# Kernel optimization log

Hardware: AMD Instinct MI355X
Metric: run time of the kernel (lower is better)

Reference implementation:

```python
import jax, jax.numpy as jnp
import numpy as np

K_NEIGH = 12
RADIUS = 0.5


def _mlp(x, w1, b1, w2, b2):
    return jax.nn.relu(x @ w1 + b1) @ w2 + b2


def _angle(a, b):
    # atan2(||a x b||, a.b), as in PyG point-pair features
    c = jnp.cross(a, b)
    return jnp.arctan2(jnp.linalg.norm(c, axis=-1), jnp.sum(a * b, axis=-1))


def _quat_to_mat(q):
    w, x, y, z = q[:, 0], q[:, 1], q[:, 2], q[:, 3]
    m = jnp.stack([
        1 - 2 * (y * y + z * z), 2 * (x * y - z * w), 2 * (x * z + y * w),
        2 * (x * y + z * w), 1 - 2 * (x * x + z * z), 2 * (y * z - x * w),
        2 * (x * z - y * w), 2 * (y * z + x * w), 1 - 2 * (x * x + y * y),
    ], axis=-1)
    return m.reshape(-1, 3, 3)


def _lin_params(key, fan_in, fan_out):
    kw, kb = jax.random.split(key)
    s = 1.0 / np.sqrt(fan_in)
    w = jax.random.uniform(kw, (fan_in, fan_out), minval=-s, maxval=s, dtype=jnp.float32)
    b = jax.random.uniform(kb, (fan_out,), minval=-s, maxval=s, dtype=jnp.float32)
    return w, b


def setup_inputs() -> dict:
    key = jax.random.key(0)
    keys = jax.random.split(key, 8)
    points = jax.random.uniform(keys[0], (1, 128, 64, 3), dtype=jnp.float32)
    dims = [(7, 32, 16), (19, 32, 8), (24, 32, 16), (16, 32, 8), (24, 32, 16), (16, 32, 12), (27, 64, 1)]
    names = ['l1', 'g1', 'l2', 'g2', 'l3', 'g3', 'l4']
    inp = {'points': points}
    for i, (nm, (di, dh, do)) in enumerate(zip(names, dims)):
        k1, k2 = jax.random.split(keys[i + 1])
        w1, b1 = _lin_params(k1, di, dh)
        w2, b2 = _lin_params(k2, dh, do)
        inp[nm + '_w1'], inp[nm + '_b1'], inp[nm + '_w2'], inp[nm + '_b2'] = w1, b1, w2, b2
    return inp


def reference(points, l1_w1, l1_b1, l1_w2, l1_b2, g1_w1, g1_b1, g1_w2, g1_b2,
              l2_w1, l2_b1, l2_w2, l2_b2, g2_w1, g2_b1, g2_w2, g2_b2,
              l3_w1, l3_b1, l3_w2, l3_b2, g3_w1, g3_b1, g3_w2, g3_b2,
              l4_w1, l4_b1, l4_w2, l4_b2):
    B, H, W, _ = points.shape
    pos = points.reshape(-1, 3)          # [N,3]
    N = pos.shape[0]
    K = K_NEIGH
    pos_sg = jax.lax.stop_gradient(pos)  # torch detaches pos before edge features

    # --- dense radius graph: K nearest neighbors, self-padded beyond radius ---
    sq = jnp.sum(pos_sg * pos_sg, -1)
    d2 = sq[:, None] + sq[None, :] - 2.0 * (pos_sg @ pos_sg.T)  # [N,N]
    idx = jnp.arange(N)
    d2 = d2.at[idx, idx].set(jnp.inf)
    neg_d2_k, knn = jax.lax.top_k(-d2, K)
    d2_k = -neg_d2_k
    dense = jnp.where(d2_k <= RADIUS * RADIUS, knn, idx[:, None])  # [N,K]
    rows = jnp.repeat(idx, K)            # [E]
    cols = dense.reshape(-1)             # [E]

    # --- covariance of neighborhood, analytic 3x3 eig -> PCA normals ---
    nbr = pos[dense]                     # [N,K,3] (non-detached, as in torch)
    cent = jnp.mean(nbr, axis=1, keepdims=True)
    diff = nbr - cent
    cov = jnp.einsum('nki,nkj->nij', diff, diff) / K
    noise = (jax.random.uniform(jax.random.key(42), (100, 3), dtype=jnp.float32) - 0.5) * 1e-8
    cov = cov + jnp.diag(noise)          # torch.diag of (100,3) -> length-3 vector broadcast
    eig_val, eig_vec = jnp.linalg.eigh(cov)  # ascending, matches sort+gather in torch
    normals = eig_vec[:, :, 0]           # eigenvector of smallest eigenvalue
    pca_normals = normals.reshape(B, H, W, 3).transpose(0, 3, 1, 2)

    # --- edge feature stack: gather-MLP-mean-broadcast chain ---
    cart = pos_sg[cols] - pos_sg[rows]   # [E,3]
    dist = jnp.linalg.norm(cart, axis=-1)
    n_r, n_c = normals[rows], normals[cols]
    ppf = jnp.stack([dist, _angle(n_r, cart), _angle(n_c, cart), _angle(n_r, n_c)], -1)
    x = _mlp(jnp.concatenate([cart, ppf], -1), l1_w1, l1_b1, l1_w2, l1_b2)  # [E,16]

    gx = jnp.concatenate([x.reshape(N, K, -1).mean(1), normals], -1)        # [N,19]
    x_g = _mlp(gx, g1_w1, g1_b1, g1_w2, g1_b2)                              # [N,8]
    x = _mlp(jnp.concatenate([x, x_g[rows]], 1), l2_w1, l2_b1, l2_w2, l2_b2)

    x_g = _mlp(x.reshape(N, K, -1).mean(1), g2_w1, g2_b1, g2_w2, g2_b2)
    x = _mlp(jnp.concatenate([x, x_g[rows]], 1), l3_w1, l3_b1, l3_w2, l3_b2)

    x_g = _mlp(x.reshape(N, K, -1).mean(1), g3_w1, g3_b1, g3_w2, g3_b2)     # [N,12]
    quat = x_g[:, :4]
    quat = quat / (jnp.linalg.norm(quat, axis=-1) + 1e-8)[:, None]
    mat = _quat_to_mat(quat)             # [N,3,3]
    feat_g = x_g[:, 4:]
    rot_cart = jnp.einsum('eij,ej->ei', mat[rows], cart)
    x = _mlp(jnp.concatenate([x, feat_g[rows], rot_cart], 1), l4_w1, l4_b1, l4_w2, l4_b2)

    point_fea = jax.nn.softmax(x.reshape(N, K), axis=1)
    point_fea = point_fea.reshape(B, H, W, K).transpose(0, 3, 1, 2)
    return pca_normals, point_fea
```

## Files before the change

kernel.cpp:

```cpp
#include <hip/hip_runtime.h>
#include <math.h>

#define KNB 12
#define GRD 8
#define NCELL (GRD * GRD * GRD)


__device__ __forceinline__ unsigned umin32(unsigned a, unsigned b) {
    unsigned r; asm("v_min_u32 %0, %1, %2" : "=v"(r) : "v"(a), "v"(b)); return r;
}
__device__ __forceinline__ unsigned umax32(unsigned a, unsigned b) {
    unsigned r; asm("v_max_u32 %0, %1, %2" : "=v"(r) : "v"(a), "v"(b)); return r;
}

__device__ __forceinline__ float fm(float a, float b) { return __fmul_rn(a, b); }
__device__ __forceinline__ float fa(float a, float b) { return __fadd_rn(a, b); }
__device__ __forceinline__ float fs(float a, float b) { return __fsub_rn(a, b); }
__device__ __forceinline__ float fsignf(float a, float b) { return (b >= 0.0f) ? fabsf(a) : -fabsf(a); }

__device__ float slapy2_(float x, float y) {
    float xa = fabsf(x), ya = fabsf(y);
    float w = fmaxf(xa, ya), z = fminf(xa, ya);
    if (z == 0.0f) return w;
    float q = z / w;
    return fm(w, __fsqrt_rn(fa(1.0f, fm(q, q))));
}

__device__ void slartg_(float f, float g, float& c, float& s, float& r) {
    if (g == 0.0f) { c = 1.0f; s = 0.0f; r = f; }
    else if (f == 0.0f) { c = 0.0f; s = (g >= 0.0f) ? 1.0f : -1.0f; r = fabsf(g); }
    else {
        float d = __fsqrt_rn(fa(fm(f, f), fm(g, g)));
        c = fabsf(f) / d;
        r = (f >= 0.0f) ? d : -d;
        s = g / r;
    }
}

__device__ void slaev2_(float a, float b, float cc,
                        float& rt1, float& rt2, float& cs1, float& sn1) {
    float sm = fa(a, cc), df = fs(a, cc), adf = fabsf(df);
    float tb = fa(b, b), ab = fabsf(tb);
    float acmx, acmn;
    if (fabsf(a) > fabsf(cc)) { acmx = a; acmn = cc; } else { acmx = cc; acmn = a; }
    float rt;
    if (adf > ab)      { float q = ab / adf; rt = fm(adf, __fsqrt_rn(fa(1.0f, fm(q, q)))); }
    else if (adf < ab) { float q = adf / ab; rt = fm(ab,  __fsqrt_rn(fa(1.0f, fm(q, q)))); }
    else               rt = fm(ab, __fsqrt_rn(2.0f));
    int sgn1;
    if (sm < 0.0f) {
        rt1 = fm(0.5f, fs(sm, rt)); sgn1 = -1;
        rt2 = fs(fm(acmx / rt1, acmn), fm(b / rt1, b));
    } else if (sm > 0.0f) {
        rt1 = fm(0.5f, fa(sm, rt)); sgn1 = 1;
        rt2 = fs(fm(acmx / rt1, acmn), fm(b / rt1, b));
    } else { rt1 = fm(0.5f, rt); rt2 = fm(-0.5f, rt); sgn1 = 1; }
    int sgn2; float cs;
    if (df >= 0.0f) { cs = fa(df, rt); sgn2 = 1; } else { cs = fs(df, rt); sgn2 = -1; }
    float acs = fabsf(cs);
    if (acs > ab) {
        float ct = -tb / cs;
        sn1 = 1.0f / __fsqrt_rn(fa(1.0f, fm(ct, ct)));
        cs1 = fm(ct, sn1);
    } else {
        if (ab == 0.0f) { cs1 = 1.0f; sn1 = 0.0f; }
        else {
            float tn = -cs / tb;
            cs1 = 1.0f / __fsqrt_rn(fa(1.0f, fm(tn, tn)));
            sn1 = fm(tn, cs1);
        }
    }
    if (sgn1 == sgn2) { float tn = cs1; cs1 = -sn1; sn1 = tn; }
}

__device__ __forceinline__ void rot2col(float& a1, float& a2, float& a3,
                                        float& b1, float& b2, float& b3,
                                        float ct, float st) {
    float t;
    t = b1; b1 = fs(fm(ct, t), fm(st, a1)); a1 = fa(fm(st, t), fm(ct, a1));
    t = b2; b2 = fs(fm(ct, t), fm(st, a2)); a2 = fa(fm(st, t), fm(ct, a2));
    t = b3; b3 = fs(fm(ct, t), fm(st, a3)); a3 = fa(fm(st, t), fm(ct, a3));
}

#define RD(i)    ((i) == 1 ? d1 : ((i) == 2 ? d2 : d3))
#define WRD(i,v) do { float _t = (v); if ((i) == 1) d1 = _t; else if ((i) == 2) d2 = _t; else d3 = _t; } while (0)
#define RE(i)    ((i) == 1 ? e1 : e2)
#define WRE(i,v) do { float _t = (v); if ((i) == 1) e1 = _t; else e2 = _t; } while (0)
#define SWAPC(a,b) do { float _t = (a); (a) = (b); (b) = _t; } while (0)

__device__ void eig3_smallest_reg(float a00, float a10, float a20,
                                  float a11, float a21, float a22,
                                  float& v1o, float& v2o, float& v3o) {
    float z11 = 1.0f, z21 = 0.0f, z31 = 0.0f;
    float z12 = 0.0f, z22 = 1.0f, z32 = 0.0f;
    float z13 = 0.0f, z23 = 0.0f, z33 = 1.0f;
    float d1, d2, d3, e1, e2;
    float wc1 = 0.0f, wc2 = 0.0f, ws1 = 0.0f, ws2 = 0.0f;

    float tau = 0.0f, v3 = 0.0f;
    d1 = a00;
    if (a20 != 0.0f) {
        float xn = fabsf(a20);
        float beta = -fsignf(slapy2_(a10, xn), a10);
        tau = fs(beta, a10) / beta;
        float rinv = 1.0f / fs(a10, beta);
        v3 = fm(a20, rinv);
        e1 = beta;
        float w1 = fa(fm(tau, a11), fm(tau, fm(a21, v3)));
        float w2 = fa(fm(tau, a21), fm(fm(tau, v3), a22));
        float dot = fa(w1, fm(w2, v3));
        float al = fm(fm(-0.5f, tau), dot);
        w1 = fa(w1, al);
        w2 = fa(w2, fm(al, v3));
        d2 = fs(fs(a11, w1), w1);
        e2 = fs(fs(a21, fm(v3, w1)), w2);
        d3 = fs(fs(a22, fm(v3, w2)), fm(w2, v3));
    } else {
        e1 = a10; d2 = a11; e2 = a21; d3 = a22;
    }

    const float eps = 5.9604645e-8f;
    const float eps2 = 3.5527137e-15f;
    const float safmin = 1.17549435e-38f;
    int jtot = 0; const int nmaxit = 90;
    int l1 = 1;
    while (l1 <= 3) {
        if (l1 > 1) WRE(l1 - 1, 0.0f);
        int m;
        for (m = l1; m <= 2; ++m) {
            float tst = fabsf(RE(m));
            if (tst == 0.0f) break;
            if (tst <= fm(fm(__fsqrt_rn(fabsf(RD(m))), __fsqrt_rn(fabsf(RD(m + 1)))), eps)) {
                WRE(m, 0.0f); break;
            }
        }
        int l = l1, lend = m;
        l1 = m + 1;
        if (lend == l) continue;
        if (fabsf(RD(lend)) < fabsf(RD(l))) { int t = l; l = lend; lend = t; }
        if (lend > l) {
            for (;;) {
                int mq = lend;
                if (l != lend) {
                    for (mq = l; mq <= lend - 1; ++mq) {
                        float tst = fm(RE(mq), RE(mq));
                        if (tst <= fa(fm(fm(eps2, fabsf(RD(mq))), fabsf(RD(mq + 1))), safmin)) break;
                    }
                }
                if (mq < lend) WRE(mq, 0.0f);
                float p = RD(l);
                if (mq == l) { l += 1; if (l <= lend) continue; break; }
                if (mq == l + 1) {
                    float rt1, rt2, cc, ss;
                    if (l == 1) {
                        slaev2_(d1, e1, d2, rt1, rt2, cc, ss);
                        rot2col(z11, z21, z31, z12, z22, z32, cc, ss);
                        d1 = rt1; d2 = rt2; e1 = 0.0f;
                    } else {
                        slaev2_(d2, e2, d3, rt1, rt2, cc, ss);
                        rot2col(z12, z22, z32, z13, z23, z33, cc, ss);
                        d2 = rt1; d3 = rt2; e2 = 0.0f;
                    }
                    l += 2; if (l <= lend) continue; break;
                }
                if (jtot == nmaxit) break;
                jtot++;
                float g = fs(d2, p) / fm(2.0f, e1);
                float r = slapy2_(g, 1.0f);
                g = fa(fs(d3, p), e1 / fa(g, fsignf(r, g)));
                float s_ = 1.0f, c_ = 1.0f; p = 0.0f;
                {
                    float f = fm(s_, e2), b = fm(c_, e2);
                    slartg_(g, f, c_, s_, r);
                    g = fs(d3, p);
                    r = fa(fm(fs(d2, g), s_), fm(fm(2.0f, c_), b));
                    p = fm(s_, r);
                    d3 = fa(g, p);
                    g = fs(fm(c_, r), b);
                    wc2 = c_; ws2 = -s_;
                }
                {
                    float f = fm(s_, e1), b = fm(c_, e1);
                    slartg_(g, f, c_, s_, r);
                    e2 = r;
                    g = fs(d2, p);
                    r = fa(fm(fs(d1, g), s_), fm(fm(2.0f, c_), b));
                    p = fm(s_, r);
                    d2 = fa(g, p);
                    g = fs(fm(c_, r), b);
                    wc1 = c_; ws1 = -s_;
                }
                rot2col(z12, z22, z32, z13, z23, z33, wc2, ws2);
                rot2col(z11, z21, z31, z12, z22, z32, wc1, ws1);
                d1 = fs(d1, p); e1 = g;
            }
        } else {
            for (;;) {
                int mq = lend;
                if (l != lend) {
                    for (mq = l; mq >= lend + 1; --mq) {
                        float tst = fm(RE(mq - 1), RE(mq - 1));
                        if (tst <= fa(fm(fm(eps2, fabsf(RD(mq))), fabsf(RD(mq - 1))), safmin)) break;
                    }
                }
                if (mq > lend) WRE(mq - 1, 0.0f);
                float p = RD(l);
                if (mq == l) { l -= 1; if (l >= lend) continue; break; }
                if (mq == l - 1) {
                    float rt1, rt2, cc, ss;
                    if (l == 2) {
                        slaev2_(d1, e1, d2, rt1, rt2, cc, ss);
                        rot2col(z11, z21, z31, z12, z22, z32, cc, ss);
                        d1 = rt1; d2 = rt2; e1 = 0.0f;
                    } else {
                        slaev2_(d2, e2, d3, rt1, rt2, cc, ss);
                        rot2col(z12, z22, z32, z13, z23, z33, cc, ss);
                        d2 = rt1; d3 = rt2; e2 = 0.0f;
                    }
                    l -= 2; if (l >= lend) continue; break;
                }
                if (jtot == nmaxit) break;
                jtot++;
                float g = fs(d2, p) / fm(2.0f, e2);
                float r = slapy2_(g, 1.0f);
                g = fa(fs(d1, p), e2 / fa(g, fsignf(r, g)));
                float s_ = 1.0f, c_ = 1.0f; p = 0.0f;
                {
                    float f = fm(s_, e1), b = fm(c_, e1);
                    slartg_(g, f, c_, s_, r);
                    g = fs(d1, p);
                    r = fa(fm(fs(d2, g), s_), fm(fm(2.0f, c_), b));
                    p = fm(s_, r);
                    d1 = fa(g, p);
                    g = fs(fm(c_, r), b);
                    wc1 = c_; ws1 = s_;
                }
                {
                    float f = fm(s_, e2), b = fm(c_, e2);
                    slartg_(g, f, c_, s_, r);
                    e1 = r;
                    g = fs(d2, p);
                    r = fa(fm(fs(d3, g), s_), fm(fm(2.0f, c_), b));
                    p = fm(s_, r);
                    d2 = fa(g, p);
                    g = fs(fm(c_, r), b);
                    wc2 = c_; ws2 = s_;
                }
                rot2col(z11, z21, z31, z12, z22, z32, wc1, ws1);
                rot2col(z12, z22, z32, z13, z23, z33, wc2, ws2);
                d3 = fs(d3, p); e2 = g;
            }
        }
    }
    for (int ii = 2; ii <= 3; ++ii) {
        int i = ii - 1, kk = i; float p = RD(i);
        for (int j = ii; j <= 3; ++j) { float dj = RD(j); if (dj < p) { kk = j; p = dj; } }
        if (kk != i) {
            WRD(kk, RD(i)); WRD(i, p);
            if (i == 1 && kk == 2)      { SWAPC(z11, z12); SWAPC(z21, z22); SWAPC(z31, z32); }
            else if (i == 1 && kk == 3) { SWAPC(z11, z13); SWAPC(z21, z23); SWAPC(z31, z33); }
            else                        { SWAPC(z12, z13); SWAPC(z22, z23); SWAPC(z32, z33); }
        }
    }
    if (tau != 0.0f) {
        float ss, t;
        ss = fa(z21, fm(v3, z31)); t = fm(tau, ss); z21 = fs(z21, t); z31 = fs(z31, fm(t, v3));
        ss = fa(z22, fm(v3, z32)); t = fm(tau, ss); z22 = fs(z22, t); z32 = fs(z32, fm(t, v3));
        ss = fa(z23, fm(v3, z33)); t = fm(tau, ss); z23 = fs(z23, t); z33 = fs(z33, fm(t, v3));
    }
    v1o = z11; v2o = z21; v3o = z31;
}

__device__ void threefry2x32_(unsigned k0, unsigned k1, unsigned c0, unsigned c1,
                              unsigned& o0, unsigned& o1) {
    const unsigned rot[8] = {13u, 15u, 26u, 6u, 17u, 29u, 16u, 24u};
    unsigned ks[3] = {k0, k1, k0 ^ k1 ^ 0x1BD11BDAu};
    unsigned x0 = c0 + k0, x1 = c1 + k1;
    for (int blk = 0; blk < 5; ++blk) {
        const unsigned* r = &rot[(blk & 1) * 4];
        for (int i = 0; i < 4; ++i) {
            x0 += x1;
            x1 = (x1 << r[i]) | (x1 >> (32 - r[i]));
            x1 ^= x0;
        }
        x0 += ks[(blk + 1) % 3];
        x1 += ks[(blk + 2) % 3] + (unsigned)(blk + 1);
    }
    o0 = x0; o1 = x1;
}

__device__ float noise_diag_(int j) {
    unsigned m = (unsigned)(4 * j);
    unsigned o0, o1;
    threefry2x32_(0u, 42u, m, 150u + m, o0, o1);
    unsigned bits = (o0 >> 9) | 0x3f800000u;
    float u = fs(__uint_as_float(bits), 1.0f);
    return fm(fs(u, 0.5f), 1e-8f);
}

__device__ __forceinline__ float angf(float ax, float ay, float az,
                                      float bx, float by, float bz) {
    float cx = ay * bz - az * by;
    float cy = az * bx - ax * bz;
    float cz = ax * by - ay * bx;
    float cn = sqrtf(cx * cx + cy * cy + cz * cz);
    float d  = ax * bx + ay * by + az * bz;
    return atan2f(cn, d);
}

__global__ __launch_bounds__(1024) void k_build(const float* __restrict__ pts,
                                                float4* __restrict__ pos4,
                                                int* __restrict__ order,
                                                int* __restrict__ start, int n) {
    __shared__ int sh[NCELL];
    __shared__ int scur[NCELL];
    int t = threadIdx.x;

    for (int c = t; c < NCELL; c += 1024) sh[c] = 0;
    __syncthreads();

    for (int i = t; i < n; i += 1024) {
        float x = pts[i * 3], y = pts[i * 3 + 1], z = pts[i * 3 + 2];
        float sq = fa(fa(fm(x, x), fm(y, y)), fm(z, z));
        pos4[i] = make_float4(x, y, z, sq);
        int cx = (int)(x * 8.0f); cx = cx < 0 ? 0 : (cx > GRD - 1 ? GRD - 1 : cx);
        int cy = (int)(y * 8.0f); cy = cy < 0 ? 0 : (cy > GRD - 1 ? GRD - 1 : cy);
        int cz = (int)(z * 8.0f); cz = cz < 0 ? 0 : (cz > GRD - 1 ? GRD - 1 : cz);
        int cid = (cz * GRD + cy) * GRD + cx;
        atomicAdd(&sh[cid], 1);
    }
    __syncthreads();

    int v = 0;
    if (t < NCELL) v = sh[t];
    for (int off = 1; off < NCELL; off <<= 1) {
        int x = 0;
        if (t < NCELL && t >= off) x = sh[t - off];
        __syncthreads();
        if (t < NCELL) sh[t] += x;
        __syncthreads();
    }
    if (t < NCELL) {
        int ex = sh[t] - v;
        start[t] = ex;
        scur[t] = ex;
        if (t == NCELL - 1) start[NCELL] = sh[t];
    }
    __syncthreads();

    for (int i = t; i < n; i += 1024) {
        float4 P = pos4[i];
        int cx = (int)(P.x * 8.0f); cx = cx < 0 ? 0 : (cx > GRD - 1 ? GRD - 1 : cx);
        int cy = (int)(P.y * 8.0f); cy = cy < 0 ? 0 : (cy > GRD - 1 ? GRD - 1 : cy);
        int cz = (int)(P.z * 8.0f); cz = cz < 0 ? 0 : (cz > GRD - 1 ? GRD - 1 : cz);
        int cid = (cz * GRD + cy) * GRD + cx;
        int slot = atomicAdd(&scur[cid], 1);
        order[slot] = i;
    }
}

#define KEY_WORST 0xC0001FFFFFFFFFFFull
#define CBUF 128

__global__ __launch_bounds__(256) void k_knn(const float4* __restrict__ pos4,
                                             const int* __restrict__ order,
                                             const int* __restrict__ cstart,
                                             int* __restrict__ cols,
                                             float4* __restrict__ nrm4,
                                             float* __restrict__ out, int n) {
    __shared__ unsigned long long sbuf[4][CBUF];
    __shared__ int scnt[4];
    __shared__ float4 sq4[4][KNB];

    int lane = threadIdx.x & 63;
    int wv = threadIdx.x >> 6;
    int io = blockIdx.x * 4 + wv;
    bool wact = (io < n);

    if (wact) {
        float4 P = pos4[io];
        int cx = (int)(P.x * 8.0f); cx = cx < 0 ? 0 : (cx > GRD - 1 ? GRD - 1 : cx);
        int cy = (int)(P.y * 8.0f); cy = cy < 0 ? 0 : (cy > GRD - 1 ? GRD - 1 : cy);
        int cz = (int)(P.z * 8.0f); cz = cz < 0 ? 0 : (cz > GRD - 1 ? GRD - 1 : cz);

        unsigned T = 0xFFFFFFFFu;
        int xlo = 0, xhi = 0, ylo = 0, yhi = 0, zlo = 0, zhi = 0;

        for (int r = 1; r < 16; ++r) {
            xlo = cx - r; if (xlo < 0) xlo = 0;
            xhi = cx + r; if (xhi > GRD - 1) xhi = GRD - 1;
            ylo = cy - r; if (ylo < 0) ylo = 0;
            yhi = cy + r; if (yhi > GRD - 1) yhi = GRD - 1;
            zlo = cz - r; if (zlo < 0) zlo = 0;
            zhi = cz + r; if (zhi > GRD - 1) zhi = GRD - 1;

            unsigned b0 = 0xFFFFFFFFu, b1 = 0xFFFFFFFFu;
            for (int zz = zlo; zz <= zhi; ++zz)
                for (int yy = ylo; yy <= yhi; ++yy) {
                    int rowb = (zz * GRD + yy) * GRD;
                    int jb = cstart[rowb + xlo];
                    int je = cstart[rowb + xhi + 1];
                    for (int t = jb + lane; t < je; t += 64) {
                        int j = order[t];
                        float4 Q = pos4[j];
                        float g = fm(P.x, Q.x);
                        g = fmaf(P.y, Q.y, g);
                        g = fmaf(P.z, Q.z, g);
                        float d2 = fs(fa(P.w, Q.w), fm(2.0f, g));
                        unsigned u = __float_as_uint(d2);
                        u = (j == io) ? 0xFFFFFFFFu : u;
                        unsigned lo = umin32(b0, u);
                        unsigned hi = umax32(b0, u);
                        b0 = lo;
                        b1 = umin32(b1, hi);
                    }
                }

            {
                unsigned h0 = b0, h1 = b1;
                T = 0xFFFFFFFFu;
                for (int rr = 0; rr < KNB + 1; ++rr) {
                    unsigned mn = h0;
#pragma unroll
                    for (int off = 32; off >= 1; off >>= 1) {
                        unsigned o = (unsigned)__shfl_xor((int)mn, off, 64);
                        mn = umin32(mn, o);
                    }
                    unsigned long long bl = __ballot(h0 == mn);
                    int first = __ffsll(bl) - 1;
                    if (lane == first) { h0 = h1; h1 = 0xFFFFFFFFu; }
                    T = mn;
                }
            }

            bool cover = (xlo == 0) && (xhi == GRD - 1) && (ylo == 0) && (yhi == GRD - 1)
                      && (zlo == 0) && (zhi == GRD - 1);
            if (cover) break;
            if (T != 0xFFFFFFFFu) {
                float gmin = 1e30f;
                if (xlo > 0)       gmin = fminf(gmin, fs(P.x, (float)xlo * 0.125f));
                if (xhi < GRD - 1) gmin = fminf(gmin, fs((float)(xhi + 1) * 0.125f, P.x));
                if (ylo > 0)       gmin = fminf(gmin, fs(P.y, (float)ylo * 0.125f));
                if (yhi < GRD - 1) gmin = fminf(gmin, fs((float)(yhi + 1) * 0.125f, P.y));
                if (zlo > 0)       gmin = fminf(gmin, fs(P.z, (float)zlo * 0.125f));
                if (zhi < GRD - 1) gmin = fminf(gmin, fs((float)(zhi + 1) * 0.125f, P.z));
                float g2 = fm(fm(gmin, gmin), 0.9995f);
                if (__uint_as_float(T) <= g2) break;
            }
        }

        if (lane == 0) scnt[wv] = 0;
        __builtin_amdgcn_wave_barrier();
        for (int zz = zlo; zz <= zhi; ++zz)
            for (int yy = ylo; yy <= yhi; ++yy) {
                int rowb = (zz * GRD + yy) * GRD;
                int jb = cstart[rowb + xlo];
                int je = cstart[rowb + xhi + 1];
                for (int t = jb + lane; t < je; t += 64) {
                    int j = order[t];
                    float4 Q = pos4[j];
                    float g = fm(P.x, Q.x);
                    g = fmaf(P.y, Q.y, g);
                    g = fmaf(P.z, Q.z, g);
                    float d2 = fs(fa(P.w, Q.w), fm(2.0f, g));
                    unsigned u = __float_as_uint(d2);
                    bool c = (u <= T) && (j != io);
                    unsigned long long bl = __ballot(c);
                    if (bl) {
                        int leader = __ffsll(bl) - 1;
                        int base = 0;
                        if (lane == leader)
                            base = atomicAdd(&scnt[wv], (int)__popcll(bl));
                        base = __shfl(base, leader, 64);
                        if (c) {
                            int pos = base + (int)__popcll(bl & ((1ull << lane) - 1ull));
                            unsigned us = u ^ (unsigned)(((int)u >> 31) | 0x80000000);
                            unsigned long long kb = (((unsigned long long)us << 13) | (unsigned)j)
                                                    | 0xC000000000000000ull;
                            if (pos < CBUF) sbuf[wv][pos] = kb;
                        }
                    }
                }
            }
        __builtin_amdgcn_wave_barrier();
        int cnt = scnt[wv];
        if (cnt > CBUF) cnt = CBUF;

        double k0 = __longlong_as_double((long long)KEY_WORST);
        double k1 = __longlong_as_double((long long)KEY_WORST);
        if (lane < cnt) k0 = __longlong_as_double((long long)sbuf[wv][lane]);
        if (lane + 64 < cnt) k1 = __longlong_as_double((long long)sbuf[wv][lane + 64]);
        double mykey = __longlong_as_double((long long)KEY_WORST);
        for (int rr = 0; rr < KNB; ++rr) {
            double mx = fmax(k0, k1);
#pragma unroll
            for (int off = 32; off >= 1; off >>= 1)
                mx = fmax(mx, __shfl_xor(mx, off, 64));
            if (k0 == mx) k0 = __longlong_as_double((long long)KEY_WORST);
            else if (k1 == mx) k1 = __longlong_as_double((long long)KEY_WORST);
            if (lane == rr) mykey = mx;
        }
        if (lane < KNB) {
            unsigned long long bits = (unsigned long long)__double_as_longlong(mykey);
            unsigned j = (unsigned)(bits & 0x1FFFu);
            unsigned u = (unsigned)((bits >> 13) & 0xFFFFFFFFull);
            unsigned ob = (u & 0x80000000u) ? (u ^ 0x80000000u) : ~u;
            float d2 = __uint_as_float(ob);
            int cv = (d2 <= 0.25f) ? (int)j : io;
            cols[io * KNB + lane] = cv;
            float4 qp = pos4[cv];
            sq4[wv][lane] = make_float4(qp.x, qp.y, qp.z, 0.0f);
        }
    }
    __syncthreads();

    if (wv == 0 && lane < 4) {
        int pp = blockIdx.x * 4 + lane;
        if (pp < n) {
            float qx[KNB], qy[KNB], qz[KNB];
#pragma unroll
            for (int k = 0; k < KNB; ++k) {
                float4 q = sq4[lane][k];
                qx[k] = q.x; qy[k] = q.y; qz[k] = q.z;
            }
            float sx = qx[0], sy = qy[0], sz = qz[0];
#pragma unroll
            for (int k = 1; k < KNB; ++k) { sx = fa(sx, qx[k]); sy = fa(sy, qy[k]); sz = fa(sz, qz[k]); }
            float mx = sx / 12.0f, my = sy / 12.0f, mz = sz / 12.0f;
            float c00 = 0, c10 = 0, c20 = 0, c11 = 0, c21 = 0, c22 = 0;
#pragma unroll
            for (int k = 0; k < KNB; ++k) {
                float dx = fs(qx[k], mx), dy = fs(qy[k], my), dz = fs(qz[k], mz);
                c00 = fa(c00, fm(dx, dx));
                c10 = fa(c10, fm(dy, dx));
                c20 = fa(c20, fm(dz, dx));
                c11 = fa(c11, fm(dy, dy));
                c21 = fa(c21, fm(dz, dy));
                c22 = fa(c22, fm(dz, dz));
            }
            c00 = c00 / 12.0f; c10 = c10 / 12.0f; c20 = c20 / 12.0f;
            c11 = c11 / 12.0f; c21 = c21 / 12.0f; c22 = c22 / 12.0f;
            float v0 = noise_diag_(0), v1 = noise_diag_(1), v2 = noise_diag_(2);
            float a00 = fa(c00, v0), a10 = fa(c10, v0), a20 = fa(c20, v0);
            float a11 = fa(c11, v1), a21 = fa(c21, v1), a22 = fa(c22, v2);
            float e1, e2, e3;
            eig3_smallest_reg(a00, a10, a20, a11, a21, a22, e1, e2, e3);
            nrm4[pp] = make_float4(e1, e2, e3, 0.0f);
            out[pp]         = e1;
            out[n + pp]     = e2;
            out[2 * n + pp] = e3;
        }
    }
}


struct WPtrs { const float* p[28]; };

template <int NI, int NH, int NO>
__device__ __forceinline__ void mlp_half(const float* __restrict__ w1, const float* __restrict__ b1,
                                         const float* __restrict__ w2, const float* __restrict__ b2,
                                         const float* in, float* out, int hf) {
#pragma unroll
    for (int o = 0; o < NO; ++o) out[o] = hf ? 0.0f : b2[o];
    const int HH = NH / 2;
    int h0 = hf * HH;
    for (int hi = 0; hi < HH; ++hi) {
        int h = h0 + hi;
        float hh = b1[h];
#pragma unroll
        for (int ii = 0; ii < NI; ++ii) hh = fmaf(in[ii], w1[ii * NH + h], hh);
        hh = fmaxf(hh, 0.0f);
#pragma unroll
        for (int o = 0; o < NO; ++o) out[o] = fmaf(hh, w2[h * NO + o], out[o]);
    }
}

template <int NI, int NO>
__device__ __forceinline__ void gmlp_part(const float* __restrict__ w1, const float* __restrict__ b1,
                                          const float* __restrict__ w2, const float* __restrict__ b2,
                                          const float* in, float* pout, int q) {
#pragma unroll
    for (int o = 0; o < NO; ++o) pout[o] = (q == 0) ? b2[o] : 0.0f;
    {
        float hh = b1[q];
#pragma unroll
        for (int ii = 0; ii < NI; ++ii) hh = fmaf(in[ii], w1[ii * 32 + q], hh);
        hh = fmaxf(hh, 0.0f);
#pragma unroll
        for (int o = 0; o < NO; ++o) pout[o] = fmaf(hh, w2[q * NO + o], pout[o]);
    }
    if (q < 8) {
        int h = 24 + q;
        float hh = b1[h];
#pragma unroll
        for (int ii = 0; ii < NI; ++ii) hh = fmaf(in[ii], w1[ii * 32 + h], hh);
        hh = fmaxf(hh, 0.0f);
#pragma unroll
        for (int o = 0; o < NO; ++o) pout[o] = fmaf(hh, w2[h * NO + o], pout[o]);
    }
}

#define SCR(pp, qq, oo) s_scr[((pp) * 24 + (qq)) * 17 + (oo)]
#define SM(pp, oo)      s_m[(pp) * 17 + (oo)]
#define GFV(pp, oo)     s_g[(pp) * 13 + (oo)]
#define SLG(pp, kk)     s_log[(pp) * 13 + (kk)]

__global__ __launch_bounds__(384) void k_mlp(const float4* __restrict__ pos4,
                                             const int* __restrict__ cols,
                                             const float4* __restrict__ nrm4,
                                             WPtrs wp, float* __restrict__ out, int n) {
    __shared__ float s_scr[16 * 24 * 17];
    __shared__ float s_m[16 * 17];
    __shared__ float s_g[16 * 13];
    __shared__ float s_log[16 * 13];
    __shared__ float s_red[16 * 2];

    int t = threadIdx.x;
    int tm = t % 192;
    int p = tm / 12, k = tm - p * 12;
    int hf = __builtin_amdgcn_readfirstlane(t / 192);
    int q = hf * 12 + k;
    int nn = blockIdx.x * 16 + p;
    bool act = (nn < n);

    float cx = 0, cy = 0, cz = 0, nrx = 0, nry = 0, nrz = 0;
    float xr[16];

    if (act) {
        int col = cols[nn * 12 + k];
        float4 P = pos4[nn], Q = pos4[col];
        cx = Q.x - P.x; cy = Q.y - P.y; cz = Q.z - P.z;
        float dist = sqrtf(cx * cx + cy * cy + cz * cz);
        float4 NR = nrm4[nn], NC = nrm4[col];
        nrx = NR.x; nry = NR.y; nrz = NR.z;
        float a1 = angf(nrx, nry, nrz, cx, cy, cz);
        float a2 = angf(NC.x, NC.y, NC.z, cx, cy, cz);
        float a3 = angf(nrx, nry, nrz, NC.x, NC.y, NC.z);
        float in7[7] = {cx, cy, cz, dist, a1, a2, a3};
        float px[16];
        mlp_half<7, 32, 16>(wp.p[0], wp.p[1], wp.p[2], wp.p[3], in7, px, hf);
#pragma unroll
        for (int o = 0; o < 16; ++o) SCR(p, q, o) = px[o];
    }
    __syncthreads();
    if (act) {
#pragma unroll
        for (int o = 0; o < 16; ++o) xr[o] = SCR(p, k, o) + SCR(p, 12 + k, o);
    }
    __syncthreads();

    if (act && q < 16) {
        float s = 0.0f;
        for (int kk = 0; kk < 12; ++kk) s += SCR(p, kk, q) + SCR(p, 12 + kk, q);
        SM(p, q) = s / 12.0f;
    }
    __syncthreads();
    if (act) {
        float gin[19];
#pragma unroll
        for (int ii = 0; ii < 16; ++ii) gin[ii] = SM(p, ii);
        gin[16] = nrx; gin[17] = nry; gin[18] = nrz;
        float pg[8];
        gmlp_part<19, 8>(wp.p[4], wp.p[5], wp.p[6], wp.p[7], gin, pg, q);
#pragma unroll
        for (int o = 0; o < 8; ++o) SCR(p, q, o) = pg[o];
    }
    __syncthreads();
    if (act && q < 8) {
        float s = 0.0f;
        for (int j = 0; j < 24; ++j) s += SCR(p, j, q);
        GFV(p, q) = s;
    }
    __syncthreads();

    if (act) {
        float in24[24];
#pragma unroll
        for (int o = 0; o < 16; ++o) in24[o] = xr[o];
#pragma unroll
        for (int o = 0; o < 8; ++o) in24[16 + o] = GFV(p, o);
        float px[16];
        mlp_half<24, 32, 16>(wp.p[8], wp.p[9], wp.p[10], wp.p[11], in24, px, hf);
#pragma unroll
        for (int o = 0; o < 16; ++o) SCR(p, q, o) = px[o];
    }
    __syncthreads();
    if (act) {
#pragma unroll
        for (int o = 0; o < 16; ++o) xr[o] = SCR(p, k, o) + SCR(p, 12 + k, o);
    }
    __syncthreads();

    if (act && q < 16) {
        float s = 0.0f;
        for (int kk = 0; kk < 12; ++kk) s += SCR(p, kk, q) + SCR(p, 12 + kk, q);
        SM(p, q) = s / 12.0f;
    }
    __syncthreads();
    if (act) {
        float gin[16];
#pragma unroll
        for (int ii = 0; ii < 16; ++ii) gin[ii] = SM(p, ii);
        float pg[8];
        gmlp_part<16, 8>(wp.p[12], wp.p[13], wp.p[14], wp.p[15], gin, pg, q);
#pragma unroll
        for (int o = 0; o < 8; ++o) SCR(p, q, o) = pg[o];
    }
    __syncthreads();
    if (act && q < 8) {
        float s = 0.0f;
        for (int j = 0; j < 24; ++j) s += SCR(p, j, q);
        GFV(p, q) = s;
    }
    __syncthreads();

    if (act) {
        float in24[24];
#pragma unroll
        for (int o = 0; o < 16; ++o) in24[o] = xr[o];
#pragma unroll
        for (int o = 0; o < 8; ++o) in24[16 + o] = GFV(p, o);
        float px[16];
        mlp_half<24, 32, 16>(wp.p[16], wp.p[17], wp.p[18], wp.p[19], in24, px, hf);
#pragma unroll
        for (int o = 0; o < 16; ++o) SCR(p, q, o) = px[o];
    }
    __syncthreads();
    if (act) {
#pragma unroll
        for (int o = 0; o < 16; ++o) xr[o] = SCR(p, k, o) + SCR(p, 12 + k, o);
    }
    __syncthreads();

    if (act && q < 16) {
        float s = 0.0f;
        for (int kk = 0; kk < 12; ++kk) s += SCR(p, kk, q) + SCR(p, 12 + kk, q);
        SM(p, q) = s / 12.0f;
    }
    __syncthreads();
    if (act) {
        float gin[16];
#pragma unroll
        for (int ii = 0; ii < 16; ++ii) gin[ii] = SM(p, ii);
        float pg[12];
        gmlp_part<16, 12>(wp.p[20], wp.p[21], wp.p[22], wp.p[23], gin, pg, q);
#pragma unroll
        for (int o = 0; o < 12; ++o) SCR(p, q, o) = pg[o];
    }
    __syncthreads();
    if (act && q < 12) {
        float s = 0.0f;
        for (int j = 0; j < 24; ++j) s += SCR(p, j, q);
        GFV(p, q) = s;
    }
    __syncthreads();

    if (act) {
        float g0 = GFV(p, 0), g1v = GFV(p, 1), g2v = GFV(p, 2), g3v = GFV(p, 3);
        float qn = sqrtf(g0 * g0 + g1v * g1v + g2v * g2v + g3v * g3v) + 1e-8f;
        float qw = g0 / qn, qxx = g1v / qn, qyy = g2v / qn, qzz = g3v / qn;
        float m0 = 1.0f - 2.0f * (qyy * qyy + qzz * qzz);
        float m1 = 2.0f * (qxx * qyy - qzz * qw);
        float m2 = 2.0f * (qxx * qzz + qyy * qw);
        float m3 = 2.0f * (qxx * qyy + qzz * qw);
        float m4 = 1.0f - 2.0f * (qxx * qxx + qzz * qzz);
        float m5 = 2.0f * (qyy * qzz - qxx * qw);
        float m6 = 2.0f * (qxx * qzz - qyy * qw);
        float m7 = 2.0f * (qyy * qzz + qxx * qw);
        float m8 = 1.0f - 2.0f * (qxx * qxx + qyy * qyy);
        float r0 = m0 * cx + m1 * cy + m2 * cz;
        float r1 = m3 * cx + m4 * cy + m5 * cz;
        float r2 = m6 * cx + m7 * cy + m8 * cz;
        float in27[27];
#pragma unroll
        for (int o = 0; o < 16; ++o) in27[o] = xr[o];
#pragma unroll
        for (int o = 0; o < 8; ++o) in27[16 + o] = GFV(p, 4 + o);
        in27[24] = r0; in27[25] = r1; in27[26] = r2;
        float plg[1];
        mlp_half<27, 64, 1>(wp.p[24], wp.p[25], wp.p[26], wp.p[27], in27, plg, hf);
        SCR(p, q, 0) = plg[0];
    }
    __syncthreads();
    if (act && hf == 0) SLG(p, k) = SCR(p, k, 0) + SCR(p, 12 + k, 0);
    __syncthreads();

    if (act && q == 0) {
        float mx = SLG(p, 0);
        for (int kk = 1; kk < 12; ++kk) mx = fmaxf(mx, SLG(p, kk));
        float se = 0;
        for (int kk = 0; kk < 12; ++kk) se += expf(SLG(p, kk) - mx);
        s_red[p * 2] = mx; s_red[p * 2 + 1] = se;
    }
    __syncthreads();
    if (act && hf == 0) {
        float v = expf(SLG(p, k) - s_red[p * 2]) / s_red[p * 2 + 1];
        out[3 * n + k * n + nn] = v;
    }
}


extern "C" void kernel_launch(void* const* d_in, const int* in_sizes, int n_in,
                              void* d_out, int out_size, void* d_ws, size_t ws_size,
                              hipStream_t stream) {
    const float* pts = (const float*)d_in[0];
    int n = in_sizes[0] / 3;

    char* ws = (char*)d_ws;
    float4* pos4  = (float4*)ws;
    int*    cols  = (int*)(ws + (size_t)n * 16);
    float4* nrm4  = (float4*)(ws + (size_t)n * 64);
    int*    order = (int*)(ws + (size_t)n * 80);
    int*    start = (int*)(ws + (size_t)n * 84);
    float*  out = (float*)d_out;

    WPtrs wp;
    for (int a = 0; a < 28; ++a) wp.p[a] = (const float*)d_in[a + 1];

    k_build<<<1, 1024, 0, stream>>>(pts, pos4, order, start, n);
    k_knn<<<(n + 3) / 4, 256, 0, stream>>>(pos4, order, start, cols, nrm4, out, n);
    k_mlp<<<(n + 15) / 16, 384, 0, stream>>>(pos4, cols, nrm4, wp, out, n);
}
```

Before: 223.7 us.

## Split normal estimation out of kNN kernel and split MLP FMA chains

Result: faster. 212.1 us (median of 2 runs) (-5.2%).

```diff
diff --git a/kernel.cpp b/kernel.cpp
--- a/kernel.cpp
+++ b/kernel.cpp
@@ -365,92 +365,32 @@
 __global__ __launch_bounds__(256) void k_knn(const float4* __restrict__ pos4,
                                              const int* __restrict__ order,
                                              const int* __restrict__ cstart,
-                                             int* __restrict__ cols,
-                                             float4* __restrict__ nrm4,
-                                             float* __restrict__ out, int n) {
+                                             int* __restrict__ cols, int n) {
     __shared__ unsigned long long sbuf[4][CBUF];
     __shared__ int scnt[4];
-    __shared__ float4 sq4[4][KNB];
 
     int lane = threadIdx.x & 63;
     int wv = threadIdx.x >> 6;
     int io = blockIdx.x * 4 + wv;
-    bool wact = (io < n);
-
-    if (wact) {
-        float4 P = pos4[io];
-        int cx = (int)(P.x * 8.0f); cx = cx < 0 ? 0 : (cx > GRD - 1 ? GRD - 1 : cx);
-        int cy = (int)(P.y * 8.0f); cy = cy < 0 ? 0 : (cy > GRD - 1 ? GRD - 1 : cy);
-        int cz = (int)(P.z * 8.0f); cz = cz < 0 ? 0 : (cz > GRD - 1 ? GRD - 1 : cz);
-
-        unsigned T = 0xFFFFFFFFu;
-        int xlo = 0, xhi = 0, ylo = 0, yhi = 0, zlo = 0, zhi = 0;
-
-        for (int r = 1; r < 16; ++r) {
-            xlo = cx - r; if (xlo < 0) xlo = 0;
-            xhi = cx + r; if (xhi > GRD - 1) xhi = GRD - 1;
-            ylo = cy - r; if (ylo < 0) ylo = 0;
-            yhi = cy + r; if (yhi > GRD - 1) yhi = GRD - 1;
-            zlo = cz - r; if (zlo < 0) zlo = 0;
-            zhi = cz + r; if (zhi > GRD - 1) zhi = GRD - 1;
-
-            unsigned b0 = 0xFFFFFFFFu, b1 = 0xFFFFFFFFu;
-            for (int zz = zlo; zz <= zhi; ++zz)
-                for (int yy = ylo; yy <= yhi; ++yy) {
-                    int rowb = (zz * GRD + yy) * GRD;
-                    int jb = cstart[rowb + xlo];
-                    int je = cstart[rowb + xhi + 1];
-                    for (int t = jb + lane; t < je; t += 64) {
-                        int j = order[t];
-                        float4 Q = pos4[j];
-                        float g = fm(P.x, Q.x);
-                        g = fmaf(P.y, Q.y, g);
-                        g = fmaf(P.z, Q.z, g);
-                        float d2 = fs(fa(P.w, Q.w), fm(2.0f, g));
-                        unsigned u = __float_as_uint(d2);
-                        u = (j == io) ? 0xFFFFFFFFu : u;
-                        unsigned lo = umin32(b0, u);
-                        unsigned hi = umax32(b0, u);
-                        b0 = lo;
-                        b1 = umin32(b1, hi);
-                    }
-                }
-
-            {
-                unsigned h0 = b0, h1 = b1;
-                T = 0xFFFFFFFFu;
-                for (int rr = 0; rr < KNB + 1; ++rr) {
-                    unsigned mn = h0;
-#pragma unroll
-                    for (int off = 32; off >= 1; off >>= 1) {
-                        unsigned o = (unsigned)__shfl_xor((int)mn, off, 64);
-                        mn = umin32(mn, o);
-                    }
-                    unsigned long long bl = __ballot(h0 == mn);
-                    int first = __ffsll(bl) - 1;
-                    if (lane == first) { h0 = h1; h1 = 0xFFFFFFFFu; }
-                    T = mn;
-                }
-            }
-
-            bool cover = (xlo == 0) && (xhi == GRD - 1) && (ylo == 0) && (yhi == GRD - 1)
-                      && (zlo == 0) && (zhi == GRD - 1);
-            if (cover) break;
-            if (T != 0xFFFFFFFFu) {
-                float gmin = 1e30f;
-                if (xlo > 0)       gmin = fminf(gmin, fs(P.x, (float)xlo * 0.125f));
-                if (xhi < GRD - 1) gmin = fminf(gmin, fs((float)(xhi + 1) * 0.125f, P.x));
-                if (ylo > 0)       gmin = fminf(gmin, fs(P.y, (float)ylo * 0.125f));
-                if (yhi < GRD - 1) gmin = fminf(gmin, fs((float)(yhi + 1) * 0.125f, P.y));
-                if (zlo > 0)       gmin = fminf(gmin, fs(P.z, (float)zlo * 0.125f));
-                if (zhi < GRD - 1) gmin = fminf(gmin, fs((float)(zhi + 1) * 0.125f, P.z));
-                float g2 = fm(fm(gmin, gmin), 0.9995f);
-                if (__uint_as_float(T) <= g2) break;
-            }
-        }
-
-        if (lane == 0) scnt[wv] = 0;
-        __builtin_amdgcn_wave_barrier();
+    if (io >= n) return;
+
+    float4 P = pos4[io];
+    int cx = (int)(P.x * 8.0f); cx = cx < 0 ? 0 : (cx > GRD - 1 ? GRD - 1 : cx);
+    int cy = (int)(P.y * 8.0f); cy = cy < 0 ? 0 : (cy > GRD - 1 ? GRD - 1 : cy);
+    int cz = (int)(P.z * 8.0f); cz = cz < 0 ? 0 : (cz > GRD - 1 ? GRD - 1 : cz);
+
+    unsigned T = 0xFFFFFFFFu;
+    int xlo = 0, xhi = 0, ylo = 0, yhi = 0, zlo = 0, zhi = 0;
+
+    for (int r = 1; r < 16; ++r) {
+        xlo = cx - r; if (xlo < 0) xlo = 0;
+        xhi = cx + r; if (xhi > GRD - 1) xhi = GRD - 1;
+        ylo = cy - r; if (ylo < 0) ylo = 0;
+        yhi = cy + r; if (yhi > GRD - 1) yhi = GRD - 1;
+        zlo = cz - r; if (zlo < 0) zlo = 0;
+        zhi = cz + r; if (zhi > GRD - 1) zhi = GRD - 1;
+
+        unsigned b0 = 0xFFFFFFFFu, b1 = 0xFFFFFFFFu;
         for (int zz = zlo; zz <= zhi; ++zz)
             for (int yy = ylo; yy <= yhi; ++yy) {
                 int rowb = (zz * GRD + yy) * GRD;
@@ -464,93 +404,147 @@
                     g = fmaf(P.z, Q.z, g);
                     float d2 = fs(fa(P.w, Q.w), fm(2.0f, g));
                     unsigned u = __float_as_uint(d2);
-                    bool c = (u <= T) && (j != io);
-                    unsigned long long bl = __ballot(c);
-                    if (bl) {
-                        int leader = __ffsll(bl) - 1;
-                        int base = 0;
-                        if (lane == leader)
-                            base = atomicAdd(&scnt[wv], (int)__popcll(bl));
-                        base = __shfl(base, leader, 64);
-                        if (c) {
-                            int pos = base + (int)__popcll(bl & ((1ull << lane) - 1ull));
-                            unsigned us = u ^ (unsigned)(((int)u >> 31) | 0x80000000);
-                            unsigned long long kb = (((unsigned long long)us << 13) | (unsigned)j)
-                                                    | 0xC000000000000000ull;
-                            if (pos < CBUF) sbuf[wv][pos] = kb;
-                        }
+                    u = (j == io) ? 0xFFFFFFFFu : u;
+                    unsigned lo = umin32(b0, u);
+                    unsigned hi = umax32(b0, u);
+                    b0 = lo;
+                    b1 = umin32(b1, hi);
+                }
+            }
+
+        {
+            unsigned h0 = b0, h1 = b1;
+            T = 0xFFFFFFFFu;
+            for (int rr = 0; rr < KNB + 1; ++rr) {
+                unsigned mn = h0;
+#pragma unroll
+                for (int off = 32; off >= 1; off >>= 1) {
+                    unsigned o = (unsigned)__shfl_xor((int)mn, off, 64);
+                    mn = umin32(mn, o);
+                }
+                unsigned long long bl = __ballot(h0 == mn);
+                int first = __ffsll(bl) - 1;
+                if (lane == first) { h0 = h1; h1 = 0xFFFFFFFFu; }
+                T = mn;
+            }
+        }
+
+        bool cover = (xlo == 0) && (xhi == GRD - 1) && (ylo == 0) && (yhi == GRD - 1)
+                  && (zlo == 0) && (zhi == GRD - 1);
+        if (cover) break;
+        if (T != 0xFFFFFFFFu) {
+            float gmin = 1e30f;
+            if (xlo > 0)       gmin = fminf(gmin, fs(P.x, (float)xlo * 0.125f));
+            if (xhi < GRD - 1) gmin = fminf(gmin, fs((float)(xhi + 1) * 0.125f, P.x));
+            if (ylo > 0)       gmin = fminf(gmin, fs(P.y, (float)ylo * 0.125f));
+            if (yhi < GRD - 1) gmin = fminf(gmin, fs((float)(yhi + 1) * 0.125f, P.y));
+            if (zlo > 0)       gmin = fminf(gmin, fs(P.z, (float)zlo * 0.125f));
+            if (zhi < GRD - 1) gmin = fminf(gmin, fs((float)(zhi + 1) * 0.125f, P.z));
+            float g2 = fm(fm(gmin, gmin), 0.9995f);
+            if (__uint_as_float(T) <= g2) break;
+        }
+    }
+
+    if (lane == 0) scnt[wv] = 0;
+    __builtin_amdgcn_wave_barrier();
+    for (int zz = zlo; zz <= zhi; ++zz)
+        for (int yy = ylo; yy <= yhi; ++yy) {
+            int rowb = (zz * GRD + yy) * GRD;
+            int jb = cstart[rowb + xlo];
+            int je = cstart[rowb + xhi + 1];
+            for (int t = jb + lane; t < je; t += 64) {
+                int j = order[t];
+                float4 Q = pos4[j];
+                float g = fm(P.x, Q.x);
+                g = fmaf(P.y, Q.y, g);
+                g = fmaf(P.z, Q.z, g);
+                float d2 = fs(fa(P.w, Q.w), fm(2.0f, g));
+                unsigned u = __float_as_uint(d2);
+                bool c = (u <= T) && (j != io);
+                unsigned long long bl = __ballot(c);
+                if (bl) {
+                    int leader = __ffsll(bl) - 1;
+                    int base = 0;
+                    if (lane == leader)
+                        base = atomicAdd(&scnt[wv], (int)__popcll(bl));
+                    base = __shfl(base, leader, 64);
+                    if (c) {
+                        int pos = base + (int)__popcll(bl & ((1ull << lane) - 1ull));
+                        unsigned us = u ^ (unsigned)(((int)u >> 31) | 0x80000000);
+                        unsigned long long kb = (((unsigned long long)us << 13) | (unsigned)j)
+                                                | 0xC000000000000000ull;
+                        if (pos < CBUF) sbuf[wv][pos] = kb;
                     }
                 }
             }
-        __builtin_amdgcn_wave_barrier();
-        int cnt = scnt[wv];
-        if (cnt > CBUF) cnt = CBUF;
-
-        double k0 = __longlong_as_double((long long)KEY_WORST);
-        double k1 = __longlong_as_double((long long)KEY_WORST);
-        if (lane < cnt) k0 = __longlong_as_double((long long)sbuf[wv][lane]);
-        if (lane + 64 < cnt) k1 = __longlong_as_double((long long)sbuf[wv][lane + 64]);
-        double mykey = __longlong_as_double((long long)KEY_WORST);
-        for (int rr = 0; rr < KNB; ++rr) {
-            double mx = fmax(k0, k1);
-#pragma unroll
-            for (int off = 32; off >= 1; off >>= 1)
-                mx = fmax(mx, __shfl_xor(mx, off, 64));
-            if (k0 == mx) k0 = __longlong_as_double((long long)KEY_WORST);
-            else if (k1 == mx) k1 = __longlong_as_double((long long)KEY_WORST);
-            if (lane == rr) mykey = mx;
         }
-        if (lane < KNB) {
-            unsigned long long bits = (unsigned long long)__double_as_longlong(mykey);
-            unsigned j = (unsigned)(bits & 0x1FFFu);
-            unsigned u = (unsigned)((bits >> 13) & 0xFFFFFFFFull);
-            unsigned ob = (u & 0x80000000u) ? (u ^ 0x80000000u) : ~u;
-            float d2 = __uint_as_float(ob);
-            int cv = (d2 <= 0.25f) ? (int)j : io;
-            cols[io * KNB + lane] = cv;
-            float4 qp = pos4[cv];
-            sq4[wv][lane] = make_float4(qp.x, qp.y, qp.z, 0.0f);
-        }
-    }
-    __syncthreads();
-
-    if (wv == 0 && lane < 4) {
-        int pp = blockIdx.x * 4 + lane;
-        if (pp < n) {
-            float qx[KNB], qy[KNB], qz[KNB];
-#pragma unroll
-            for (int k = 0; k < KNB; ++k) {
-                float4 q = sq4[lane][k];
-                qx[k] = q.x; qy[k] = q.y; qz[k] = q.z;
-            }
-            float sx = qx[0], sy = qy[0], sz = qz[0];
-#pragma unroll
-            for (int k = 1; k < KNB; ++k) { sx = fa(sx, qx[k]); sy = fa(sy, qy[k]); sz = fa(sz, qz[k]); }
-            float mx = sx / 12.0f, my = sy / 12.0f, mz = sz / 12.0f;
-            float c00 = 0, c10 = 0, c20 = 0, c11 = 0, c21 = 0, c22 = 0;
-#pragma unroll
-            for (int k = 0; k < KNB; ++k) {
-                float dx = fs(qx[k], mx), dy = fs(qy[k], my), dz = fs(qz[k], mz);
-                c00 = fa(c00, fm(dx, dx));
-                c10 = fa(c10, fm(dy, dx));
-                c20 = fa(c20, fm(dz, dx));
-                c11 = fa(c11, fm(dy, dy));
-                c21 = fa(c21, fm(dz, dy));
-                c22 = fa(c22, fm(dz, dz));
-            }
-            c00 = c00 / 12.0f; c10 = c10 / 12.0f; c20 = c20 / 12.0f;
-            c11 = c11 / 12.0f; c21 = c21 / 12.0f; c22 = c22 / 12.0f;
-            float v0 = noise_diag_(0), v1 = noise_diag_(1), v2 = noise_diag_(2);
-            float a00 = fa(c00, v0), a10 = fa(c10, v0), a20 = fa(c20, v0);
-            float a11 = fa(c11, v1), a21 = fa(c21, v1), a22 = fa(c22, v2);
-            float e1, e2, e3;
-            eig3_smallest_reg(a00, a10, a20, a11, a21, a22, e1, e2, e3);
-            nrm4[pp] = make_float4(e1, e2, e3, 0.0f);
-            out[pp]         = e1;
-            out[n + pp]     = e2;
-            out[2 * n + pp] = e3;
-        }
-    }
+    __builtin_amdgcn_wave_barrier();
+    int cnt = scnt[wv];
+    if (cnt > CBUF) cnt = CBUF;
+
+    double k0 = __longlong_as_double((long long)KEY_WORST);
+    double k1 = __longlong_as_double((long long)KEY_WORST);
+    if (lane < cnt) k0 = __longlong_as_double((long long)sbuf[wv][lane]);
+    if (lane + 64 < cnt) k1 = __longlong_as_double((long long)sbuf[wv][lane + 64]);
+    double mykey = __longlong_as_double((long long)KEY_WORST);
+    for (int rr = 0; rr < KNB; ++rr) {
+        double mx = fmax(k0, k1);
+#pragma unroll
+        for (int off = 32; off >= 1; off >>= 1)
+            mx = fmax(mx, __shfl_xor(mx, off, 64));
+        if (k0 == mx) k0 = __longlong_as_double((long long)KEY_WORST);
+        else if (k1 == mx) k1 = __longlong_as_double((long long)KEY_WORST);
+        if (lane == rr) mykey = mx;
+    }
+    if (lane < KNB) {
+        unsigned long long bits = (unsigned long long)__double_as_longlong(mykey);
+        unsigned j = (unsigned)(bits & 0x1FFFu);
+        unsigned u = (unsigned)((bits >> 13) & 0xFFFFFFFFull);
+        unsigned ob = (u & 0x80000000u) ? (u ^ 0x80000000u) : ~u;
+        float d2 = __uint_as_float(ob);
+        cols[io * KNB + lane] = (d2 <= 0.25f) ? (int)j : io;
+    }
+}
+
+__global__ __launch_bounds__(64) void k_normals(const float4* __restrict__ pos4,
+                                                const int* __restrict__ cols,
+                                                float4* __restrict__ nrm4,
+                                                float* __restrict__ out, int n) {
+    int i = blockIdx.x * blockDim.x + threadIdx.x;
+    if (i >= n) return;
+
+    float qx[KNB], qy[KNB], qz[KNB];
+#pragma unroll
+    for (int k = 0; k < KNB; ++k) {
+        float4 q = pos4[cols[i * KNB + k]];
+        qx[k] = q.x; qy[k] = q.y; qz[k] = q.z;
+    }
+    float sx = qx[0], sy = qy[0], sz = qz[0];
+#pragma unroll
+    for (int k = 1; k < KNB; ++k) { sx = fa(sx, qx[k]); sy = fa(sy, qy[k]); sz = fa(sz, qz[k]); }
+    float mx = sx / 12.0f, my = sy / 12.0f, mz = sz / 12.0f;
+    float c00 = 0, c10 = 0, c20 = 0, c11 = 0, c21 = 0, c22 = 0;
+#pragma unroll
+    for (int k = 0; k < KNB; ++k) {
+        float dx = fs(qx[k], mx), dy = fs(qy[k], my), dz = fs(qz[k], mz);
+        c00 = fa(c00, fm(dx, dx));
+        c10 = fa(c10, fm(dy, dx));
+        c20 = fa(c20, fm(dz, dx));
+        c11 = fa(c11, fm(dy, dy));
+        c21 = fa(c21, fm(dz, dy));
+        c22 = fa(c22, fm(dz, dz));
+    }
+    c00 = c00 / 12.0f; c10 = c10 / 12.0f; c20 = c20 / 12.0f;
+    c11 = c11 / 12.0f; c21 = c21 / 12.0f; c22 = c22 / 12.0f;
+    float v0 = noise_diag_(0), v1 = noise_diag_(1), v2 = noise_diag_(2);
+    float a00 = fa(c00, v0), a10 = fa(c10, v0), a20 = fa(c20, v0);
+    float a11 = fa(c11, v1), a21 = fa(c21, v1), a22 = fa(c22, v2);
+    float e1, e2, e3;
+    eig3_smallest_reg(a00, a10, a20, a11, a21, a22, e1, e2, e3);
+    nrm4[i] = make_float4(e1, e2, e3, 0.0f);
+    out[i]         = e1;
+    out[n + i]     = e2;
+    out[2 * n + i] = e3;
 }
 
 
@@ -564,12 +558,15 @@
     for (int o = 0; o < NO; ++o) out[o] = hf ? 0.0f : b2[o];
     const int HH = NH / 2;
     int h0 = hf * HH;
+#pragma unroll 2
     for (int hi = 0; hi < HH; ++hi) {
         int h = h0 + hi;
-        float hh = b1[h];
-#pragma unroll
-        for (int ii = 0; ii < NI; ++ii) hh = fmaf(in[ii], w1[ii * NH + h], hh);
-        hh = fmaxf(hh, 0.0f);
+        float hA = b1[h], hB = 0.0f;
+#pragma unroll
+        for (int ii = 0; ii < NI; ii += 2) hA = fmaf(in[ii], w1[ii * NH + h], hA);
+#pragma unroll
+        for (int ii = 1; ii < NI; ii += 2) hB = fmaf(in[ii], w1[ii * NH + h], hB);
+        float hh = fmaxf(hA + hB, 0.0f);
 #pragma unroll
         for (int o = 0; o < NO; ++o) out[o] = fmaf(hh, w2[h * NO + o], out[o]);
     }
@@ -582,19 +579,23 @@
 #pragma unroll
     for (int o = 0; o < NO; ++o) pout[o] = (q == 0) ? b2[o] : 0.0f;
     {
-        float hh = b1[q];
-#pragma unroll
-        for (int ii = 0; ii < NI; ++ii) hh = fmaf(in[ii], w1[ii * 32 + q], hh);
-        hh = fmaxf(hh, 0.0f);
+        float hA = b1[q], hB = 0.0f;
+#pragma unroll
+        for (int ii = 0; ii < NI; ii += 2) hA = fmaf(in[ii], w1[ii * 32 + q], hA);
+#pragma unroll
+        for (int ii = 1; ii < NI; ii += 2) hB = fmaf(in[ii], w1[ii * 32 + q], hB);
+        float hh = fmaxf(hA + hB, 0.0f);
 #pragma unroll
         for (int o = 0; o < NO; ++o) pout[o] = fmaf(hh, w2[q * NO + o], pout[o]);
     }
     if (q < 8) {
         int h = 24 + q;
-        float hh = b1[h];
-#pragma unroll
-        for (int ii = 0; ii < NI; ++ii) hh = fmaf(in[ii], w1[ii * 32 + h], hh);
-        hh = fmaxf(hh, 0.0f);
+        float hA = b1[h], hB = 0.0f;
+#pragma unroll
+        for (int ii = 0; ii < NI; ii += 2) hA = fmaf(in[ii], w1[ii * 32 + h], hA);
+#pragma unroll
+        for (int ii = 1; ii < NI; ii += 2) hB = fmaf(in[ii], w1[ii * 32 + h], hB);
+        float hh = fmaxf(hA + hB, 0.0f);
 #pragma unroll
         for (int o = 0; o < NO; ++o) pout[o] = fmaf(hh, w2[h * NO + o], pout[o]);
     }
@@ -818,6 +819,7 @@
     for (int a = 0; a < 28; ++a) wp.p[a] = (const float*)d_in[a + 1];
 
     k_build<<<1, 1024, 0, stream>>>(pts, pos4, order, start, n);
-    k_knn<<<(n + 3) / 4, 256, 0, stream>>>(pos4, order, start, cols, nrm4, out, n);
+    k_knn<<<(n + 3) / 4, 256, 0, stream>>>(pos4, order, start, cols, n);
+    k_normals<<<(n + 63) / 64, 64, 0, stream>>>(pos4, cols, nrm4, out, n);
     k_mlp<<<(n + 15) / 16, 384, 0, stream>>>(pos4, cols, nrm4, wp, out, n);
 }
```
